# Performance work log

Hardware: AMD Instinct MI355X
Metric: run time of the kernel (lower is better)

## Reference

```python
import jax, jax.numpy as jnp
import numpy as np

B, T, N, CIN, H, K, HOR = 64, 12, 800, 2, 64, 3, 12
TCOV_IN, TCOV_H, MNUM, MDIM = 60, 2, 4, 8
KAPPA = 0.05
IN0 = CIN + TCOV_H  # layer-0 input dim: data channels + time-covariate embedding


def setup_inputs() -> dict:
    key = jax.random.key(0)
    ks = jax.random.split(key, 24)
    def nrm(k, shape, s=0.1):
        return jax.random.normal(k, shape, jnp.float32) * s
    inp = {}
    inp["x_seq"] = jax.random.normal(ks[0], (B, T, N, CIN), jnp.float32)
    inp["t_x"] = jax.random.normal(ks[1], (B, T, TCOV_IN), jnp.float32)
    inp["t_y"] = jax.random.normal(ks[2], (B, HOR, TCOV_IN), jnp.float32)
    # adaptive graph as in init_adp_graph: softmax(relu(v1 @ v2), axis=1)
    inp["G"] = jax.nn.softmax(jax.nn.relu(nrm(ks[3], (N, 20), 1.0) @ nrm(ks[4], (20, N), 1.0)), axis=1)
    i = 5
    for pre in ("enc", "dec"):
        for l, hin in enumerate((IN0, H)):
            inp[f"{pre}_Wg{l}"] = nrm(ks[i], ((hin + H) * K, 2 * H)); i += 1
            inp[f"{pre}_bg{l}"] = jnp.zeros((2 * H,), jnp.float32)
            inp[f"{pre}_Wc{l}"] = nrm(ks[i], ((hin + H) * K, H)); i += 1
            inp[f"{pre}_bc{l}"] = jnp.zeros((H,), jnp.float32)
    inp["mlp_W1"] = nrm(ks[i], (TCOV_IN, 10)); i += 1
    inp["mlp_b1"] = jnp.zeros((10,), jnp.float32)
    inp["mlp_W2"] = nrm(ks[i], (10, TCOV_H * N)); i += 1
    inp["mlp_b2"] = jnp.zeros((TCOV_H * N,), jnp.float32)
    inp["memory"] = nrm(ks[i], (MNUM, MDIM), 1.0); i += 1
    inp["Wa"] = nrm(ks[i], (N * H, MDIM), 0.01); i += 1
    inp["fc"] = nrm(ks[i], (MDIM, MDIM * N), 0.1); i += 1
    inp["proj_W"] = nrm(ks[i], (H + MDIM, CIN)); i += 1
    inp["proj_b"] = jnp.zeros((CIN,), jnp.float32)
    return inp


def _cheby(G):
    # Chebyshev basis T_0..T_{K-1}: T_0=I, T_1=G, T_k = 2 G T_{k-1} - T_{k-2}
    Gs = [jnp.eye(N, dtype=G.dtype), G]
    for _ in range(2, K):
        Gs.append(2.0 * (G @ Gs[-1]) - Gs[-2])
    return jnp.stack(Gs[:K])  # (K, N, N)


def _gconv(x, Gs, W, b):
    # mixhop: h_k = kappa*x + (1-kappa) * einsum('bnp,nm->bmp', x, T_k); concat over k, then project
    agg = KAPPA * x[None] + (1.0 - KAPPA) * jnp.einsum('bnp,knm->kbmp', x, Gs)  # (K,B,N,P)
    Bq, Nq, P = x.shape
    h = jnp.transpose(agg, (1, 2, 0, 3)).reshape(Bq, Nq, K * P)  # matches torch.cat order
    return h @ W + b


def _cell(x, h, Gs, Wg, bg, Wc, bc):
    # GCRU cell: graph-conv GRU
    ur = _gconv(jnp.concatenate([x, h], -1), Gs, Wg, bg)
    u, r = jnp.split(ur, 2, axis=-1)
    u = jax.nn.sigmoid(u)
    r = jax.nn.sigmoid(r)
    c = jnp.tanh(_gconv(jnp.concatenate([x, r * h], -1), Gs, Wc, bc))
    return (1.0 - u) * h + u * c


def _mlp(t, W1, b1, W2, b2):
    # nn.Sequential(Linear, Linear) -- no activation in between
    return (t @ W1 + b1) @ W2 + b2


def reference(x_seq, t_x, t_y, G, enc_Wg0, enc_bg0, enc_Wc0, enc_bc0, enc_Wg1, enc_bg1, enc_Wc1, enc_bc1, dec_Wg0, dec_bg0, dec_Wc0, dec_bc0, dec_Wg1, dec_bg1, dec_Wc1, dec_bc1, mlp_W1, mlp_b1, mlp_W2, mlp_b2, memory, Wa, fc, proj_W, proj_b):
    Gs = _cheby(G)
    # time covariates for encoder input
    tx_emb = _mlp(t_x, mlp_W1, mlp_b1, mlp_W2, mlp_b2).reshape(B, T, N, TCOV_H)
    x = jnp.concatenate([x_seq, tx_emb], -1)  # (B,T,N,IN0)
    # encoder: scan over time per layer
    seq = jnp.swapaxes(x, 0, 1)  # (T,B,N,.)
    enc_params = [(enc_Wg0, enc_bg0, enc_Wc0, enc_bc0), (enc_Wg1, enc_bg1, enc_Wc1, enc_bc1)]
    h_last = []
    for (Wg, bg, Wc, bc) in enc_params:
        def step(h, xt, Wg=Wg, bg=bg, Wc=Wc, bc=bc):
            hn = _cell(xt, h, Gs, Wg, bg, Wc, bc)
            return hn, hn
        h0 = jnp.zeros((B, N, H), x.dtype)
        hT, seq = jax.lax.scan(step, h0, seq)
        h_last.append(hT)
    dec_params = [(dec_Wg0, dec_bg0, dec_Wc0, dec_bc0), (dec_Wg1, dec_bg1, dec_Wc1, dec_bc1)]
    ty = jnp.swapaxes(t_y, 0, 1)  # (HOR,B,TCOV_IN)

    def dec_step(carry, tyt):
        go, h0, h1 = carry
        tye = _mlp(tyt, mlp_W1, mlp_b1, mlp_W2, mlp_b2).reshape(B, N, TCOV_H)
        xin = jnp.concatenate([go, tye], -1)
        h0 = _cell(xin, h0, Gs, *dec_params[0])
        h1 = _cell(h0, h1, Gs, *dec_params[1])
        # query_st_memory
        q = h1.reshape(B, N * H) @ Wa  # (B, MDIM)
        att = jax.nn.softmax(q @ memory.T, axis=1)  # (B, MNUM)
        attm = ((att @ memory) @ fc).reshape(B, N, MDIM)
        out = jax.nn.relu(jnp.concatenate([h1, attm], -1) @ proj_W + proj_b)  # (B,N,CIN)
        return (out, h0, h1), out

    go0 = jnp.zeros((B, N, CIN), x.dtype)
    _, outs = jax.lax.scan(dec_step, (go0, h_last[0], h_last[1]), ty)
    return jnp.swapaxes(outs, 0, 1)  # (B,HOR,N,CIN)
```

## Files before the change

### kernel.cpp

```cpp
#include <hip/hip_runtime.h>
#include <math.h>

typedef _Float16 f16_t;
typedef _Float16 half8 __attribute__((ext_vector_type(8)));
typedef float f32x4 __attribute__((ext_vector_type(4)));


struct Params {
  const float *x_seq, *t_x, *t_y, *G;
  const float *Wraw[8], *bia[8];
  const float *mW1, *mb1, *mW2, *mb2, *mem, *Wa, *fc, *projW, *projb;
  float* dout;
  float *h0, *h1, *txe, *tye, *hidb, *partial, *Wat;
  f16_t *T2h, *Bpk, *Y0g, *Ybg, *Y0c, *Ybc, *Uh;
  f16_t* wsp[8];
};

__device__ __forceinline__ float sigm(float x) { return 1.0f / (1.0f + expf(-x)); }

__device__ __forceinline__ int xcd_swz(int orig, int nwg) {
  int q = nwg >> 3, r = nwg & 7, xcd = orig & 7, j = orig >> 3;
  return (xcd < r ? xcd * (q + 1) : r * (q + 1) + (xcd - r) * q) + j;
}

__device__ __forceinline__ void gload16(const void* g, void* l) {
  __builtin_amdgcn_global_load_lds((const __attribute__((address_space(1))) void*)g,
                                   (__attribute__((address_space(3))) void*)l, 16, 0, 0);
}


__global__ void __launch_bounds__(256) k_pre0(Params p) {
  int nt = gridDim.x * blockDim.x, id = blockIdx.x * blockDim.x + threadIdx.x;
  float4 z = {0.f, 0.f, 0.f, 0.f};
  for (int i = id; i < 64 * 64 * 200; i += nt) { ((float4*)p.h0)[i] = z; ((float4*)p.h1)[i] = z; }
  for (int w = 0; w < 8; ++w) {
    int layer = (w >> 1) & 1, cand = w & 1;
    int P = layer ? 128 : 68, NC = cand ? 64 : 128;
    const float* W = p.Wraw[w];
    f16_t* dst = p.wsp[w];
    int tot = 3 * NC * 128;
    for (int idx = id; idx < tot; idx += nt) {
      int s = idx / (NC * 128), rem = idx - s * (NC * 128);
      int c = rem >> 7, pp = rem & 127;
      float v = 0.f;
      if (pp < P) {
        if (s == 0)
          v = W[(size_t)pp * NC + c] + 0.05f * (W[(size_t)(P + pp) * NC + c] + W[(size_t)(2 * P + pp) * NC + c]);
        else
          v = 0.95f * W[(size_t)(s * P + pp) * NC + c];
      }
      dst[idx] = (f16_t)v;
    }
  }
  for (int idx = id; idx < 15360; idx += nt) {
    int half = idx / 7680, rem = idx - half * 7680;
    int r = rem / 10, j = rem - r * 10;
    const float* tin = half ? p.t_y : p.t_x;
    float a = p.mb1[j];
    for (int k = 0; k < 60; ++k) a += tin[(size_t)r * 60 + k] * p.mW1[k * 10 + j];
    p.hidb[idx] = a;
  }
  for (int idx = id; idx < 409600; idx += nt) {
    int c = idx / 6400, r2 = idx - c * 6400;
    int n = r2 >> 3, d = r2 & 7;
    p.Wat[idx] = p.Wa[((size_t)n * 64 + c) * 8 + d];
  }
}

__global__ void __launch_bounds__(256) k_pre1(Params p) {
  __shared__ float As[16 * 68];
  __shared__ float Bs[16 * 68];
  int tid = threadIdx.x, tx = tid & 15, ty = tid >> 4;
  const float* A = p.G;
  for (int tile = blockIdx.x; tile < 169; tile += gridDim.x) {
    int bx = tile % 13, by = tile / 13;
    int rowBase = by * 64, colBase = bx * 64;
    float acc[4][4] = {};
    for (int k0 = 0; k0 < 800; k0 += 16) {
      __syncthreads();
      for (int e = tid; e < 1024; e += 256) {
        int r = e >> 4, c = e & 15;
        int gr = rowBase + r;
        As[c * 68 + r] = (gr < 800) ? A[gr * 800 + k0 + c] : 0.f;
      }
      for (int e = tid; e < 1024; e += 256) {
        int r = e >> 6, c = e & 63;
        int gc = colBase + c;
        Bs[r * 68 + c] = (gc < 800) ? A[(k0 + r) * 800 + gc] : 0.f;
      }
      __syncthreads();
#pragma unroll
      for (int kk = 0; kk < 16; ++kk) {
        float4 a4 = *(const float4*)&As[kk * 68 + ty * 4];
        float4 b4 = *(const float4*)&Bs[kk * 68 + tx * 4];
        float av[4] = {a4.x, a4.y, a4.z, a4.w};
        float bv[4] = {b4.x, b4.y, b4.z, b4.w};
#pragma unroll
        for (int i = 0; i < 4; ++i)
#pragma unroll
          for (int j = 0; j < 4; ++j) acc[i][j] += av[i] * bv[j];
      }
    }
#pragma unroll
    for (int i = 0; i < 4; ++i) {
      int m = rowBase + ty * 4 + i;
      if (m >= 800) continue;
#pragma unroll
      for (int j = 0; j < 4; ++j) {
        int n = colBase + tx * 4 + j;
        if (n < 800) p.T2h[(size_t)m * 800 + n] = (f16_t)(2.f * acc[i][j] - (m == n ? 1.f : 0.f));
      }
    }
  }
  int nt = gridDim.x * blockDim.x, id = blockIdx.x * blockDim.x + threadIdx.x;
  for (int idx = id; idx < 2 * 768 * 1600; idx += nt) {
    int half = idx / (768 * 1600), rem = idx - half * (768 * 1600);
    int r = rem / 1600, o = rem - r * 1600;
    const float* hid = p.hidb + half * 7680;
    float* emb = half ? p.tye : p.txe;
    float a = p.mb2[o];
#pragma unroll
    for (int k = 0; k < 10; ++k) a += hid[r * 10 + k] * p.mW2[k * 1600 + o];
    emb[rem] = a;
  }
}

__global__ void __launch_bounds__(256) k_pre2(Params p) {
  int nt = gridDim.x * blockDim.x, id = blockIdx.x * blockDim.x + threadIdx.x;
  for (int idx = id; idx < 7 * 50 * 4096; idx += nt) {
    int nT = idx / 204800, rem = idx - nT * 204800;
    int ks = rem >> 12, i = rem & 4095;
    int kg = i >> 10, col = (i >> 3) & 127, e = i & 7;
    int k = ks * 32 + kg * 8 + e;
    int n = nT * 128 + col;
    f16_t v = (f16_t)0.f;
    if (n < 800) v = (k < 800) ? (f16_t)p.G[(size_t)k * 800 + n] : p.T2h[(size_t)(k - 800) * 800 + n];
    p.Bpk[idx] = v;
  }
}

template <int LAYER>
__global__ void __launch_bounds__(256, 3) g_small(Params p, int widx, int dec, int t) {
  __shared__ f16_t XS[128 * 136];
  unsigned* XS32 = (unsigned*)XS;
  int tid = threadIdx.x, lane = tid & 63, wid = tid >> 6;
  int lrow = lane & 15, lgrp = lane >> 4;
  int wm = wid >> 1, wn = wid & 1;
  int swz = xcd_swz(blockIdx.x, gridDim.x);
  int b = swz / 7, nBase = (swz % 7) * 128;
  const f16_t* __restrict__ wb = p.wsp[widx];
  const float* emb = dec ? p.tye : p.txe;

  {
    int rp = tid >> 3, n0 = (tid & 7) * 16;
    int ng = nBase + n0;
    bool nval = ng < 800;
    for (int pass = 0; pass < 2; ++pass) {
      float v[2][16];
#pragma unroll
      for (int par = 0; par < 2; ++par) {
        int cp = pass * 64 + 2 * rp + par;
        float* vv = v[par];
        if (!nval) {
#pragma unroll
          for (int i = 0; i < 16; ++i) vv[i] = 0.f;
        } else if (LAYER == 1) {
          const float* src = (cp < 64) ? p.h0 + ((size_t)(b * 64 + cp)) * 800 + ng
                                       : p.h1 + ((size_t)(b * 64 + cp - 64)) * 800 + ng;
#pragma unroll
          for (int q = 0; q < 4; ++q) {
            float4 f = *(const float4*)(src + q * 4);
            vv[q * 4 + 0] = f.x; vv[q * 4 + 1] = f.y; vv[q * 4 + 2] = f.z; vv[q * 4 + 3] = f.w;
          }
        } else {
          if (cp >= 68) {
#pragma unroll
            for (int i = 0; i < 16; ++i) vv[i] = 0.f;
          } else if (cp >= 4) {
            const float* src = p.h0 + ((size_t)(b * 64 + cp - 4)) * 800 + ng;
#pragma unroll
            for (int q = 0; q < 4; ++q) {
              float4 f = *(const float4*)(src + q * 4);
              vv[q * 4 + 0] = f.x; vv[q * 4 + 1] = f.y; vv[q * 4 + 2] = f.z; vv[q * 4 + 3] = f.w;
            }
          } else if (cp >= 2) {
#pragma unroll
            for (int i = 0; i < 16; ++i)
              vv[i] = emb[(size_t)(b * 12 + t) * 1600 + (ng + i) * 2 + (cp - 2)];
          } else {
            if (dec) {
              if (t == 0) {
#pragma unroll
                for (int i = 0; i < 16; ++i) vv[i] = 0.f;
              } else {
#pragma unroll
                for (int i = 0; i < 16; ++i)
                  vv[i] = p.dout[((size_t)(b * 12 + t - 1) * 800 + ng + i) * 2 + cp];
              }
            } else {
#pragma unroll
              for (int i = 0; i < 16; ++i)
                vv[i] = p.x_seq[((size_t)(b * 12 + t) * 800 + ng + i) * 2 + cp];
            }
          }
        }
      }
#pragma unroll
      for (int i = 0; i < 16; ++i) {
        union { f16_t h[2]; unsigned u; } pk;
        pk.h[0] = (f16_t)v[0][i];
        pk.h[1] = (f16_t)v[1][i];
        XS32[(n0 + i) * 68 + pass * 32 + rp] = pk.u;
      }
    }
  }
  __syncthreads();

  for (int s = 0; s < 3; ++s) {
    f32x4 acc[4][4];
#pragma unroll
    for (int i = 0; i < 4; ++i)
#pragma unroll
      for (int j = 0; j < 4; ++j) acc[i][j] = (f32x4){0.f, 0.f, 0.f, 0.f};
#pragma unroll
    for (int ks = 0; ks < 4; ++ks) {
      half8 fa[4], fx[4];
#pragma unroll
      for (int mf = 0; mf < 4; ++mf)
        fa[mf] = *(const half8*)(wb + ((size_t)(s * 128 + wm * 64 + mf * 16 + lrow) << 7) + ks * 32 + lgrp * 8);
#pragma unroll
      for (int nt = 0; nt < 4; ++nt)
        fx[nt] = *(const half8*)(XS + (wn * 64 + nt * 16 + lrow) * 136 + ks * 32 + lgrp * 8);
#pragma unroll
      for (int mf = 0; mf < 4; ++mf)
#pragma unroll
        for (int nt = 0; nt < 4; ++nt)
          acc[mf][nt] = __builtin_amdgcn_mfma_f32_16x16x32_f16(fa[mf], fx[nt], acc[mf][nt], 0, 0, 0);
    }
#pragma unroll
    for (int mf = 0; mf < 4; ++mf)
#pragma unroll
      for (int nt = 0; nt < 4; ++nt) {
        int n = nBase + wn * 64 + nt * 16 + lrow;
        if (n >= 800) continue;
#pragma unroll
        for (int j = 0; j < 4; ++j) {
          int c = wm * 64 + mf * 16 + lgrp * 4 + j;
          size_t r = (size_t)(b * 128 + c);
          f16_t val = (f16_t)acc[mf][nt][j];
          if (s == 0) {
            p.Y0g[r * 800 + n] = val;
          } else {
            int kp = (s - 1) * 800 + n;
            p.Ybg[((size_t)(kp >> 3) * 8192 + r) * 8 + (kp & 7)] = val;
          }
        }
      }
  }
}

template <int LAYER>
__global__ void __launch_bounds__(256, 4) g_biggate(Params p, int w0, int dec, int t, float* hcur) {
  constexpr int Pin = LAYER ? 64 : 4;
  __shared__ __align__(16) f16_t SH[18432];
  f16_t* AS = SH;
  f16_t* BS = SH + 6144;
  int tid = threadIdx.x, lane = tid & 63, w = tid >> 6;
  int lrow = lane & 15, lgrp = lane >> 4;
  int wm = w >> 1, wn = w & 1;
  int swz = xcd_swz(blockIdx.x, gridDim.x);
  int rt = swz / 7;
  int rBase = rt * 64;
  int nTile = swz % 7;
  int b = rt >> 1;
  int rhblk = rt & 1;
  const f16_t* __restrict__ Abase = p.Ybg;
  const f16_t* __restrict__ Bbase = p.Bpk + (size_t)nTile * 204800;
  const float* bias = p.bia[w0];

  auto stage = [&](int buf, int ks) {
    gload16(Abase + ((size_t)(ks * 4 + w) * 8192 + rBase + lane) * 8, AS + buf * 2048 + w * 512);
    gload16(Bbase + (size_t)ks * 4096 + (size_t)(w * 2 + 0) * 512 + lane * 8, BS + buf * 4096 + (w * 2 + 0) * 512);
    gload16(Bbase + (size_t)ks * 4096 + (size_t)(w * 2 + 1) * 512 + lane * 8, BS + buf * 4096 + (w * 2 + 1) * 512);
  };

  f32x4 acc[2][4];
#pragma unroll
  for (int i = 0; i < 2; ++i)
#pragma unroll
    for (int j = 0; j < 4; ++j) acc[i][j] = (f32x4){0.f, 0.f, 0.f, 0.f};

  stage(0, 0);
  stage(1, 1);
  for (int ks = 0; ks < 50; ++ks) {
    if (ks == 49) {
      asm volatile("s_waitcnt vmcnt(0)" ::: "memory");
    } else {
      asm volatile("s_waitcnt vmcnt(3)" ::: "memory");
    }
    __builtin_amdgcn_s_barrier();
    __builtin_amdgcn_sched_barrier(0);
    if (ks + 2 < 50) stage((ks + 2) % 3, ks + 2);
    int cur = ks % 3;
    half8 fa[2], fb[4];
#pragma unroll
    for (int mt = 0; mt < 2; ++mt)
      fa[mt] = *(const half8*)(AS + cur * 2048 + lgrp * 512 + (wm * 32 + mt * 16 + lrow) * 8);
#pragma unroll
    for (int nt = 0; nt < 4; ++nt)
      fb[nt] = *(const half8*)(BS + cur * 4096 + lgrp * 1024 + (wn * 64 + nt * 16 + lrow) * 8);
#pragma unroll
    for (int mt = 0; mt < 2; ++mt)
#pragma unroll
      for (int nt = 0; nt < 4; ++nt)
        acc[mt][nt] = __builtin_amdgcn_mfma_f32_16x16x32_f16(fa[mt], fb[nt], acc[mt][nt], 0, 0, 0);
  }

  if (!rhblk) {
#pragma unroll
    for (int mt = 0; mt < 2; ++mt)
#pragma unroll
      for (int nt = 0; nt < 4; ++nt) {
        int n = nTile * 128 + wn * 64 + nt * 16 + lrow;
        if (n >= 800) continue;
#pragma unroll
        for (int j = 0; j < 4; ++j) {
          int c = wm * 32 + mt * 16 + lgrp * 4 + j;
          int r = rBase + c;
          float v = acc[mt][nt][j] + (float)p.Y0g[(size_t)r * 800 + n] + bias[c];
          p.Uh[(size_t)(b * 64 + c) * 800 + n] = (f16_t)sigm(v);
        }
      }
    return;
  }

  f16_t rhv[2][4][4];
#pragma unroll
  for (int mt = 0; mt < 2; ++mt)
#pragma unroll
    for (int nt = 0; nt < 4; ++nt) {
      int n = nTile * 128 + wn * 64 + nt * 16 + lrow;
#pragma unroll
      for (int j = 0; j < 4; ++j) {
        int jj = wm * 32 + mt * 16 + lgrp * 4 + j;
        if (n < 800) {
          int r = rBase + jj;
          float v = acc[mt][nt][j] + (float)p.Y0g[(size_t)r * 800 + n] + bias[64 + jj];
          float hv = hcur[(size_t)(b * 64 + jj) * 800 + n];
          rhv[mt][nt][j] = (f16_t)(sigm(v) * hv);
        } else {
          rhv[mt][nt][j] = (f16_t)0.f;
        }
      }
    }

  __syncthreads();
  f16_t* Xc = SH;

#pragma unroll
  for (int mt = 0; mt < 2; ++mt)
#pragma unroll
    for (int nt = 0; nt < 4; ++nt) {
      int col = wn * 64 + nt * 16 + lrow;
#pragma unroll
      for (int j = 0; j < 4; ++j) {
        int jj = wm * 32 + mt * 16 + lgrp * 4 + j;
        Xc[col * 136 + Pin + jj] = rhv[mt][nt][j];
      }
    }
  if (LAYER == 1) {
    int ct = tid >> 2, nq = tid & 3;
    const float* src = p.h0 + (size_t)(b * 64 + ct) * 800;
#pragma unroll 8
    for (int i = 0; i < 32; ++i) {
      int nl = nq * 32 + i;
      int n = nTile * 128 + nl;
      float v = (n < 800) ? src[n] : 0.f;
      Xc[nl * 136 + ct] = (f16_t)v;
    }
  } else {
    if (tid < 128) {
      int col = tid;
      int n = nTile * 128 + col;
      float v0 = 0.f, v1 = 0.f, v2 = 0.f, v3 = 0.f;
      if (n < 800) {
        if (dec) {
          if (t > 0) {
            v0 = p.dout[((size_t)(b * 12 + t - 1) * 800 + n) * 2 + 0];
            v1 = p.dout[((size_t)(b * 12 + t - 1) * 800 + n) * 2 + 1];
          }
        } else {
          v0 = p.x_seq[((size_t)(b * 12 + t) * 800 + n) * 2 + 0];
          v1 = p.x_seq[((size_t)(b * 12 + t) * 800 + n) * 2 + 1];
        }
        const float* emb = dec ? p.tye : p.txe;
        v2 = emb[(size_t)(b * 12 + t) * 1600 + n * 2 + 0];
        v3 = emb[(size_t)(b * 12 + t) * 1600 + n * 2 + 1];
      }
      Xc[col * 136 + 0] = (f16_t)v0;
      Xc[col * 136 + 1] = (f16_t)v1;
      Xc[col * 136 + 2] = (f16_t)v2;
      Xc[col * 136 + 3] = (f16_t)v3;
      unsigned* z32 = (unsigned*)(Xc + col * 136 + 68);
#pragma unroll
      for (int q = 0; q < 30; ++q) z32[q] = 0u;
    }
  }
  __syncthreads();

  const f16_t* __restrict__ wc = p.wsp[w0 + 1];
  int cwn = w;
  for (int s = 0; s < 3; ++s) {
    f32x4 ac[4][2];
#pragma unroll
    for (int i = 0; i < 4; ++i)
#pragma unroll
      for (int j = 0; j < 2; ++j) ac[i][j] = (f32x4){0.f, 0.f, 0.f, 0.f};
#pragma unroll
    for (int ks = 0; ks < 4; ++ks) {
      half8 fa[4], fx[2];
#pragma unroll
      for (int mf = 0; mf < 4; ++mf)
        fa[mf] = *(const half8*)(wc + ((size_t)(s * 64 + mf * 16 + lrow) << 7) + ks * 32 + lgrp * 8);
#pragma unroll
      for (int nt = 0; nt < 2; ++nt)
        fx[nt] = *(const half8*)(Xc + (cwn * 32 + nt * 16 + lrow) * 136 + ks * 32 + lgrp * 8);
#pragma unroll
      for (int mf = 0; mf < 4; ++mf)
#pragma unroll
        for (int nt = 0; nt < 2; ++nt)
          ac[mf][nt] = __builtin_amdgcn_mfma_f32_16x16x32_f16(fa[mf], fx[nt], ac[mf][nt], 0, 0, 0);
    }
#pragma unroll
    for (int mf = 0; mf < 4; ++mf)
#pragma unroll
      for (int nt = 0; nt < 2; ++nt) {
        int n = nTile * 128 + cwn * 32 + nt * 16 + lrow;
        if (n >= 800) continue;
#pragma unroll
        for (int j = 0; j < 4; ++j) {
          int c = mf * 16 + lgrp * 4 + j;
          size_t r = (size_t)(b * 64 + c);
          f16_t val = (f16_t)ac[mf][nt][j];
          if (s == 0) {
            p.Y0c[r * 800 + n] = val;
          } else {
            int kp = (s - 1) * 800 + n;
            p.Ybc[((size_t)(kp >> 3) * 4096 + r) * 8 + (kp & 7)] = val;
          }
        }
      }
  }
}

__global__ void __launch_bounds__(256, 4) g_bigcand(Params p, int widx, float* hcur) {
  __shared__ __align__(16) f16_t SH[18432];
  f16_t* AS = SH;
  f16_t* BS = SH + 6144;
  int tid = threadIdx.x, lane = tid & 63, w = tid >> 6;
  int lrow = lane & 15, lgrp = lane >> 4;
  int wm = w >> 1, wn = w & 1;
  int swz = xcd_swz(blockIdx.x, gridDim.x);
  int rBase = (swz / 7) * 64;
  int nTile = swz % 7;
  const f16_t* __restrict__ Abase = p.Ybc;
  const f16_t* __restrict__ Bbase = p.Bpk + (size_t)nTile * 204800;
  const float* bias = p.bia[widx];

  auto stage = [&](int buf, int ks) {
    gload16(Abase + ((size_t)(ks * 4 + w) * 4096 + rBase + lane) * 8, AS + buf * 2048 + w * 512);
    gload16(Bbase + (size_t)ks * 4096 + (size_t)(w * 2 + 0) * 512 + lane * 8, BS + buf * 4096 + (w * 2 + 0) * 512);
    gload16(Bbase + (size_t)ks * 4096 + (size_t)(w * 2 + 1) * 512 + lane * 8, BS + buf * 4096 + (w * 2 + 1) * 512);
  };

  f32x4 acc[2][4];
#pragma unroll
  for (int i = 0; i < 2; ++i)
#pragma unroll
    for (int j = 0; j < 4; ++j) acc[i][j] = (f32x4){0.f, 0.f, 0.f, 0.f};

  stage(0, 0);
  stage(1, 1);
  for (int ks = 0; ks < 50; ++ks) {
    if (ks == 49) {
      asm volatile("s_waitcnt vmcnt(0)" ::: "memory");
    } else {
      asm volatile("s_waitcnt vmcnt(3)" ::: "memory");
    }
    __builtin_amdgcn_s_barrier();
    __builtin_amdgcn_sched_barrier(0);
    if (ks + 2 < 50) stage((ks + 2) % 3, ks + 2);
    int cur = ks % 3;
    half8 fa[2], fb[4];
#pragma unroll
    for (int mt = 0; mt < 2; ++mt)
      fa[mt] = *(const half8*)(AS + cur * 2048 + lgrp * 512 + (wm * 32 + mt * 16 + lrow) * 8);
#pragma unroll
    for (int nt = 0; nt < 4; ++nt)
      fb[nt] = *(const half8*)(BS + cur * 4096 + lgrp * 1024 + (wn * 64 + nt * 16 + lrow) * 8);
#pragma unroll
    for (int mt = 0; mt < 2; ++mt)
#pragma unroll
      for (int nt = 0; nt < 4; ++nt)
        acc[mt][nt] = __builtin_amdgcn_mfma_f32_16x16x32_f16(fa[mt], fb[nt], acc[mt][nt], 0, 0, 0);
  }

#pragma unroll
  for (int mt = 0; mt < 2; ++mt)
#pragma unroll
    for (int nt = 0; nt < 4; ++nt) {
      int n = nTile * 128 + wn * 64 + nt * 16 + lrow;
      if (n >= 800) continue;
#pragma unroll
      for (int j = 0; j < 4; ++j) {
        int r = rBase + wm * 32 + mt * 16 + lgrp * 4 + j;
        int b = r >> 6, c = r & 63;
        float v = acc[mt][nt][j] + (float)p.Y0c[(size_t)r * 800 + n] + bias[c];
        float u = (float)p.Uh[(size_t)(b * 64 + c) * 800 + n];
        float hv = hcur[(size_t)(b * 64 + c) * 800 + n];
        hcur[(size_t)(b * 64 + c) * 800 + n] = (1.f - u) * hv + u * tanhf(v);
      }
    }
}


__global__ void __launch_bounds__(256) k_att1(Params p) {
  int gwid = (blockIdx.x * blockDim.x + threadIdx.x) >> 6;
  int nw = (gridDim.x * blockDim.x) >> 6;
  int lane = threadIdx.x & 63;
  for (int tile = gwid; tile < 1024; tile += nw) {
    int cx = tile & 15, b = tile >> 4;
    float acc[8] = {};
    const float* hrow = p.h1 + (size_t)b * 51200 + cx * 3200;
    const float* wbase = p.Wat + (size_t)cx * 3200 * 8;
    for (int i = lane; i < 3200; i += 64) {
      float hv = hrow[i];
      const float* wr = wbase + (size_t)i * 8;
#pragma unroll
      for (int j = 0; j < 8; ++j) acc[j] += hv * wr[j];
    }
#pragma unroll
    for (int s = 1; s < 64; s <<= 1) {
#pragma unroll
      for (int j = 0; j < 8; ++j) acc[j] += __shfl_xor(acc[j], s);
    }
    if (lane == 0) {
#pragma unroll
      for (int j = 0; j < 8; ++j) p.partial[((size_t)b * 16 + cx) * 8 + j] = acc[j];
    }
  }
}

__global__ void __launch_bounds__(256) k_att2(Params p, int t) {
  int b = blockIdx.x >> 2, q4 = blockIdx.x & 3;
  int tid = threadIdx.x;
  float qv[8] = {};
  for (int cx = 0; cx < 16; ++cx)
#pragma unroll
    for (int j = 0; j < 8; ++j) qv[j] += p.partial[((size_t)b * 16 + cx) * 8 + j];
  float sco[4], mx = -1e30f;
#pragma unroll
  for (int m = 0; m < 4; ++m) {
    float s = 0.f;
#pragma unroll
    for (int d = 0; d < 8; ++d) s += qv[d] * p.mem[m * 8 + d];
    sco[m] = s;
    mx = fmaxf(mx, s);
  }
  float se = 0.f;
#pragma unroll
  for (int m = 0; m < 4; ++m) { sco[m] = expf(sco[m] - mx); se += sco[m]; }
  float attv[8];
#pragma unroll
  for (int d = 0; d < 8; ++d) {
    float av = 0.f;
#pragma unroll
    for (int m = 0; m < 4; ++m) av += (sco[m] / se) * p.mem[m * 8 + d];
    attv[d] = av;
  }
  if (tid >= 200) return;
  int n = q4 * 200 + tid;
  float attm[8];
#pragma unroll
  for (int d = 0; d < 8; ++d) {
    float s = 0.f;
#pragma unroll
    for (int m = 0; m < 8; ++m) s += attv[m] * p.fc[(size_t)m * 6400 + n * 8 + d];
    attm[d] = s;
  }
  float o0 = p.projb[0], o1 = p.projb[1];
  const float* hb = p.h1 + (size_t)b * 51200 + n;
#pragma unroll 16
  for (int j = 0; j < 64; ++j) {
    float hv = hb[(size_t)j * 800];
    o0 += hv * p.projW[j * 2 + 0];
    o1 += hv * p.projW[j * 2 + 1];
  }
#pragma unroll
  for (int d = 0; d < 8; ++d) {
    o0 += attm[d] * p.projW[(64 + d) * 2 + 0];
    o1 += attm[d] * p.projW[(64 + d) * 2 + 1];
  }
  size_t base = ((size_t)(b * 12 + t) * 800 + n) * 2;
  p.dout[base + 0] = fmaxf(o0, 0.f);
  p.dout[base + 1] = fmaxf(o1, 0.f);
}


extern "C" void kernel_launch(void* const* d_in, const int* in_sizes, int n_in,
                              void* d_out, int out_size, void* d_ws, size_t ws_size,
                              hipStream_t stream) {
  Params P;
  P.x_seq = (const float*)d_in[0];
  P.t_x = (const float*)d_in[1];
  P.t_y = (const float*)d_in[2];
  P.G = (const float*)d_in[3];
  P.Wraw[0] = (const float*)d_in[4];  P.bia[0] = (const float*)d_in[5];
  P.Wraw[1] = (const float*)d_in[6];  P.bia[1] = (const float*)d_in[7];
  P.Wraw[2] = (const float*)d_in[8];  P.bia[2] = (const float*)d_in[9];
  P.Wraw[3] = (const float*)d_in[10]; P.bia[3] = (const float*)d_in[11];
  P.Wraw[4] = (const float*)d_in[12]; P.bia[4] = (const float*)d_in[13];
  P.Wraw[5] = (const float*)d_in[14]; P.bia[5] = (const float*)d_in[15];
  P.Wraw[6] = (const float*)d_in[16]; P.bia[6] = (const float*)d_in[17];
  P.Wraw[7] = (const float*)d_in[18]; P.bia[7] = (const float*)d_in[19];
  P.mW1 = (const float*)d_in[20];
  P.mb1 = (const float*)d_in[21];
  P.mW2 = (const float*)d_in[22];
  P.mb2 = (const float*)d_in[23];
  P.mem = (const float*)d_in[24];
  P.Wa = (const float*)d_in[25];
  P.fc = (const float*)d_in[26];
  P.projW = (const float*)d_in[27];
  P.projb = (const float*)d_in[28];
  P.dout = (float*)d_out;

  float* ws = (float*)d_ws;
  size_t off = 0;
  auto alloc = [&](size_t nel) { float* q = ws + off; off += (nel + 3) & ~(size_t)3; return q; };
  P.T2h = (f16_t*)alloc(320000);
  P.Bpk = (f16_t*)alloc((size_t)7 * 50 * 4096 / 2);
  P.Y0g = (f16_t*)alloc((size_t)8192 * 800 / 2);
  P.Ybg = (f16_t*)alloc((size_t)1600 * 8192 / 2);
  P.Y0c = (f16_t*)alloc((size_t)4096 * 800 / 2);
  P.Ybc = (f16_t*)alloc((size_t)1600 * 4096 / 2);
  P.Uh = (f16_t*)alloc((size_t)4096 * 800 / 2);
  P.h0 = alloc((size_t)4096 * 800);
  P.h1 = alloc((size_t)4096 * 800);
  P.txe = alloc((size_t)768 * 1600);
  P.tye = alloc((size_t)768 * 1600);
  P.hidb = alloc(15360);
  P.partial = alloc(8192);
  P.Wat = alloc(409600);
  for (int w = 0; w < 8; ++w) {
    int cand = w & 1;
    int NC = cand ? 64 : 128;
    P.wsp[w] = (f16_t*)alloc((size_t)3 * NC * 128 / 2);
  }

  k_pre0<<<512, 256, 0, stream>>>(P);
  k_pre1<<<512, 256, 0, stream>>>(P);
  k_pre2<<<512, 256, 0, stream>>>(P);

  auto cell = [&](int dec, int t) {
    int w0 = dec * 4;
    g_small<0><<<448, 256, 0, stream>>>(P, w0 + 0, dec, t);
    g_biggate<0><<<896, 256, 0, stream>>>(P, w0 + 0, dec, t, P.h0);
    g_bigcand<<<448, 256, 0, stream>>>(P, w0 + 1, P.h0);
    g_small<1><<<448, 256, 0, stream>>>(P, w0 + 2, dec, t);
    g_biggate<1><<<896, 256, 0, stream>>>(P, w0 + 2, dec, t, P.h1);
    g_bigcand<<<448, 256, 0, stream>>>(P, w0 + 3, P.h1);
  };

  for (int t = 0; t < 12; ++t) cell(0, t);
  for (int t = 0; t < 12; ++t) {
    cell(1, t);
    k_att1<<<256, 256, 0, stream>>>(P);
    k_att2<<<256, 256, 0, stream>>>(P, t);
  }
}
```

Baseline: 6.597 ms.

## Wavefront-pipeline encoder layers so layer 0 step s runs with layer 1 step s-1

Restructures the encoder schedule into a diagonal wavefront. Each launch now runs layer 0 at time s and layer 1 at time s-1 together, with the block index selecting the layer, and intermediate buffers are duplicated per layer so the two can run concurrently. This halves the number of encoder launches and doubles the grid size per launch, which is meant to cut launch and tail overhead and raise occupancy. The cost is double the workspace for intermediates and kernels that branch on the block index.

```diff
diff --git a/kernel.cpp b/kernel.cpp
--- a/kernel.cpp
+++ b/kernel.cpp
@@ -12,7 +12,8 @@
   const float *mW1, *mb1, *mW2, *mb2, *mem, *Wa, *fc, *projW, *projb;
   float* dout;
   float *h0, *h1, *txe, *tye, *hidb, *partial, *Wat;
-  f16_t *T2h, *Bpk, *Y0g, *Ybg, *Y0c, *Ybc, *Uh;
+  f16_t *T2h, *Bpk;
+  f16_t *Y0gL[2], *YbgL[2], *Y0cL[2], *YbcL[2], *UhL[2];
   f16_t* wsp[8];
 };
 
@@ -140,13 +141,14 @@
 }
 
 template <int LAYER>
-__global__ void __launch_bounds__(256, 3) g_small(Params p, int widx, int dec, int t) {
-  __shared__ f16_t XS[128 * 136];
-  unsigned* XS32 = (unsigned*)XS;
+__device__ void small_body(const Params& p, char* smraw, int widx, int dec, int t,
+                           f16_t* __restrict__ Y0g, f16_t* __restrict__ Ybg, int lblk) {
+  f16_t* XS = (f16_t*)smraw;
+  unsigned* XS32 = (unsigned*)smraw;
   int tid = threadIdx.x, lane = tid & 63, wid = tid >> 6;
   int lrow = lane & 15, lgrp = lane >> 4;
   int wm = wid >> 1, wn = wid & 1;
-  int swz = xcd_swz(blockIdx.x, gridDim.x);
+  int swz = xcd_swz(lblk, 448);
   int b = swz / 7, nBase = (swz % 7) * 128;
   const f16_t* __restrict__ wb = p.wsp[widx];
   const float* emb = dec ? p.tye : p.txe;
@@ -249,10 +251,10 @@
           size_t r = (size_t)(b * 128 + c);
           f16_t val = (f16_t)acc[mf][nt][j];
           if (s == 0) {
-            p.Y0g[r * 800 + n] = val;
+            Y0g[r * 800 + n] = val;
           } else {
             int kp = (s - 1) * 800 + n;
-            p.Ybg[((size_t)(kp >> 3) * 8192 + r) * 8 + (kp & 7)] = val;
+            Ybg[((size_t)(kp >> 3) * 8192 + r) * 8 + (kp & 7)] = val;
           }
         }
       }
@@ -260,26 +262,28 @@
 }
 
 template <int LAYER>
-__global__ void __launch_bounds__(256, 4) g_biggate(Params p, int w0, int dec, int t, float* hcur) {
+__device__ void biggate_body(const Params& p, char* smraw, int w0, int dec, int t, float* hcur,
+                             const f16_t* __restrict__ Y0g, const f16_t* __restrict__ Ybg,
+                             f16_t* __restrict__ Y0c, f16_t* __restrict__ Ybc,
+                             f16_t* __restrict__ Uh, int lblk) {
   constexpr int Pin = LAYER ? 64 : 4;
-  __shared__ __align__(16) f16_t SH[18432];
+  f16_t* SH = (f16_t*)smraw;
   f16_t* AS = SH;
   f16_t* BS = SH + 6144;
   int tid = threadIdx.x, lane = tid & 63, w = tid >> 6;
   int lrow = lane & 15, lgrp = lane >> 4;
   int wm = w >> 1, wn = w & 1;
-  int swz = xcd_swz(blockIdx.x, gridDim.x);
+  int swz = xcd_swz(lblk, 896);
   int rt = swz / 7;
   int rBase = rt * 64;
   int nTile = swz % 7;
   int b = rt >> 1;
   int rhblk = rt & 1;
-  const f16_t* __restrict__ Abase = p.Ybg;
   const f16_t* __restrict__ Bbase = p.Bpk + (size_t)nTile * 204800;
   const float* bias = p.bia[w0];
 
   auto stage = [&](int buf, int ks) {
-    gload16(Abase + ((size_t)(ks * 4 + w) * 8192 + rBase + lane) * 8, AS + buf * 2048 + w * 512);
+    gload16(Ybg + ((size_t)(ks * 4 + w) * 8192 + rBase + lane) * 8, AS + buf * 2048 + w * 512);
     gload16(Bbase + (size_t)ks * 4096 + (size_t)(w * 2 + 0) * 512 + lane * 8, BS + buf * 4096 + (w * 2 + 0) * 512);
     gload16(Bbase + (size_t)ks * 4096 + (size_t)(w * 2 + 1) * 512 + lane * 8, BS + buf * 4096 + (w * 2 + 1) * 512);
   };
@@ -327,8 +331,8 @@
         for (int j = 0; j < 4; ++j) {
           int c = wm * 32 + mt * 16 + lgrp * 4 + j;
           int r = rBase + c;
-          float v = acc[mt][nt][j] + (float)p.Y0g[(size_t)r * 800 + n] + bias[c];
-          p.Uh[(size_t)(b * 64 + c) * 800 + n] = (f16_t)sigm(v);
+          float v = acc[mt][nt][j] + (float)Y0g[(size_t)r * 800 + n] + bias[c];
+          Uh[(size_t)(b * 64 + c) * 800 + n] = (f16_t)sigm(v);
         }
       }
     return;
@@ -345,7 +349,7 @@
         int jj = wm * 32 + mt * 16 + lgrp * 4 + j;
         if (n < 800) {
           int r = rBase + jj;
-          float v = acc[mt][nt][j] + (float)p.Y0g[(size_t)r * 800 + n] + bias[64 + jj];
+          float v = acc[mt][nt][j] + (float)Y0g[(size_t)r * 800 + n] + bias[64 + jj];
           float hv = hcur[(size_t)(b * 64 + jj) * 800 + n];
           rhv[mt][nt][j] = (f16_t)(sigm(v) * hv);
         } else {
@@ -443,32 +447,33 @@
           size_t r = (size_t)(b * 64 + c);
           f16_t val = (f16_t)ac[mf][nt][j];
           if (s == 0) {
-            p.Y0c[r * 800 + n] = val;
+            Y0c[r * 800 + n] = val;
           } else {
             int kp = (s - 1) * 800 + n;
-            p.Ybc[((size_t)(kp >> 3) * 4096 + r) * 8 + (kp & 7)] = val;
+            Ybc[((size_t)(kp >> 3) * 4096 + r) * 8 + (kp & 7)] = val;
           }
         }
       }
   }
 }
 
-__global__ void __launch_bounds__(256, 4) g_bigcand(Params p, int widx, float* hcur) {
-  __shared__ __align__(16) f16_t SH[18432];
+__device__ void bigcand_body(const Params& p, char* smraw, int widx, float* hcur,
+                             const f16_t* __restrict__ Y0c, const f16_t* __restrict__ Ybc,
+                             const f16_t* __restrict__ Uh, int lblk) {
+  f16_t* SH = (f16_t*)smraw;
   f16_t* AS = SH;
   f16_t* BS = SH + 6144;
   int tid = threadIdx.x, lane = tid & 63, w = tid >> 6;
   int lrow = lane & 15, lgrp = lane >> 4;
   int wm = w >> 1, wn = w & 1;
-  int swz = xcd_swz(blockIdx.x, gridDim.x);
+  int swz = xcd_swz(lblk, 448);
   int rBase = (swz / 7) * 64;
   int nTile = swz % 7;
-  const f16_t* __restrict__ Abase = p.Ybc;
   const f16_t* __restrict__ Bbase = p.Bpk + (size_t)nTile * 204800;
   const float* bias = p.bia[widx];
 
   auto stage = [&](int buf, int ks) {
-    gload16(Abase + ((size_t)(ks * 4 + w) * 4096 + rBase + lane) * 8, AS + buf * 2048 + w * 512);
+    gload16(Ybc + ((size_t)(ks * 4 + w) * 4096 + rBase + lane) * 8, AS + buf * 2048 + w * 512);
     gload16(Bbase + (size_t)ks * 4096 + (size_t)(w * 2 + 0) * 512 + lane * 8, BS + buf * 4096 + (w * 2 + 0) * 512);
     gload16(Bbase + (size_t)ks * 4096 + (size_t)(w * 2 + 1) * 512 + lane * 8, BS + buf * 4096 + (w * 2 + 1) * 512);
   };
@@ -515,12 +520,52 @@
       for (int j = 0; j < 4; ++j) {
         int r = rBase + wm * 32 + mt * 16 + lgrp * 4 + j;
         int b = r >> 6, c = r & 63;
-        float v = acc[mt][nt][j] + (float)p.Y0c[(size_t)r * 800 + n] + bias[c];
-        float u = (float)p.Uh[(size_t)(b * 64 + c) * 800 + n];
+        float v = acc[mt][nt][j] + (float)Y0c[(size_t)r * 800 + n] + bias[c];
+        float u = (float)Uh[(size_t)(b * 64 + c) * 800 + n];
         float hv = hcur[(size_t)(b * 64 + c) * 800 + n];
         hcur[(size_t)(b * 64 + c) * 800 + n] = (1.f - u) * hv + u * tanhf(v);
       }
     }
+}
+
+
+template <int LAYER>
+__global__ void __launch_bounds__(256, 3) s_one(Params p, int widx, int dec, int t) {
+  __shared__ __align__(16) char sm[34816];
+  small_body<LAYER>(p, sm, widx, dec, t, p.Y0gL[LAYER], p.YbgL[LAYER], blockIdx.x);
+}
+__global__ void __launch_bounds__(256, 3) s_both(Params p, int t0, int t1) {
+  __shared__ __align__(16) char sm[34816];
+  if (blockIdx.x < 448)
+    small_body<0>(p, sm, 0, 0, t0, p.Y0gL[0], p.YbgL[0], blockIdx.x);
+  else
+    small_body<1>(p, sm, 2, 0, t1, p.Y0gL[1], p.YbgL[1], blockIdx.x - 448);
+}
+
+template <int LAYER>
+__global__ void __launch_bounds__(256, 4) gg_one(Params p, int w0, int dec, int t) {
+  __shared__ __align__(16) char sm[36864];
+  biggate_body<LAYER>(p, sm, w0, dec, t, LAYER ? p.h1 : p.h0, p.Y0gL[LAYER], p.YbgL[LAYER],
+                      p.Y0cL[LAYER], p.YbcL[LAYER], p.UhL[LAYER], blockIdx.x);
+}
+__global__ void __launch_bounds__(256, 4) gg_both(Params p, int t0, int t1) {
+  __shared__ __align__(16) char sm[36864];
+  if (blockIdx.x < 896)
+    biggate_body<0>(p, sm, 0, 0, t0, p.h0, p.Y0gL[0], p.YbgL[0], p.Y0cL[0], p.YbcL[0], p.UhL[0], blockIdx.x);
+  else
+    biggate_body<1>(p, sm, 2, 0, t1, p.h1, p.Y0gL[1], p.YbgL[1], p.Y0cL[1], p.YbcL[1], p.UhL[1], blockIdx.x - 896);
+}
+
+__global__ void __launch_bounds__(256, 4) gc_one(Params p, int widx, int layer) {
+  __shared__ __align__(16) char sm[36864];
+  bigcand_body(p, sm, widx, layer ? p.h1 : p.h0, p.Y0cL[layer], p.YbcL[layer], p.UhL[layer], blockIdx.x);
+}
+__global__ void __launch_bounds__(256, 4) gc_both(Params p) {
+  __shared__ __align__(16) char sm[36864];
+  if (blockIdx.x < 448)
+    bigcand_body(p, sm, 1, p.h0, p.Y0cL[0], p.YbcL[0], p.UhL[0], blockIdx.x);
+  else
+    bigcand_body(p, sm, 3, p.h1, p.Y0cL[1], p.YbcL[1], p.UhL[1], blockIdx.x - 448);
 }
 
 
@@ -639,11 +684,13 @@
   auto alloc = [&](size_t nel) { float* q = ws + off; off += (nel + 3) & ~(size_t)3; return q; };
   P.T2h = (f16_t*)alloc(320000);
   P.Bpk = (f16_t*)alloc((size_t)7 * 50 * 4096 / 2);
-  P.Y0g = (f16_t*)alloc((size_t)8192 * 800 / 2);
-  P.Ybg = (f16_t*)alloc((size_t)1600 * 8192 / 2);
-  P.Y0c = (f16_t*)alloc((size_t)4096 * 800 / 2);
-  P.Ybc = (f16_t*)alloc((size_t)1600 * 4096 / 2);
-  P.Uh = (f16_t*)alloc((size_t)4096 * 800 / 2);
+  for (int l = 0; l < 2; ++l) {
+    P.Y0gL[l] = (f16_t*)alloc((size_t)8192 * 800 / 2);
+    P.YbgL[l] = (f16_t*)alloc((size_t)1600 * 8192 / 2);
+    P.Y0cL[l] = (f16_t*)alloc((size_t)4096 * 800 / 2);
+    P.YbcL[l] = (f16_t*)alloc((size_t)1600 * 4096 / 2);
+    P.UhL[l] = (f16_t*)alloc((size_t)4096 * 800 / 2);
+  }
   P.h0 = alloc((size_t)4096 * 800);
   P.h1 = alloc((size_t)4096 * 800);
   P.txe = alloc((size_t)768 * 1600);
@@ -661,19 +708,25 @@
   k_pre1<<<512, 256, 0, stream>>>(P);
   k_pre2<<<512, 256, 0, stream>>>(P);
 
-  auto cell = [&](int dec, int t) {
-    int w0 = dec * 4;
-    g_small<0><<<448, 256, 0, stream>>>(P, w0 + 0, dec, t);
-    g_biggate<0><<<896, 256, 0, stream>>>(P, w0 + 0, dec, t, P.h0);
-    g_bigcand<<<448, 256, 0, stream>>>(P, w0 + 1, P.h0);
-    g_small<1><<<448, 256, 0, stream>>>(P, w0 + 2, dec, t);
-    g_biggate<1><<<896, 256, 0, stream>>>(P, w0 + 2, dec, t, P.h1);
-    g_bigcand<<<448, 256, 0, stream>>>(P, w0 + 3, P.h1);
-  };
-
-  for (int t = 0; t < 12; ++t) cell(0, t);
+  s_one<0><<<448, 256, 0, stream>>>(P, 0, 0, 0);
+  gg_one<0><<<896, 256, 0, stream>>>(P, 0, 0, 0);
+  gc_one<<<448, 256, 0, stream>>>(P, 1, 0);
+  for (int s = 1; s <= 11; ++s) {
+    s_both<<<896, 256, 0, stream>>>(P, s, s - 1);
+    gg_both<<<1792, 256, 0, stream>>>(P, s, s - 1);
+    gc_both<<<896, 256, 0, stream>>>(P);
+  }
+  s_one<1><<<448, 256, 0, stream>>>(P, 2, 0, 11);
+  gg_one<1><<<896, 256, 0, stream>>>(P, 2, 0, 11);
+  gc_one<<<448, 256, 0, stream>>>(P, 3, 1);
+
   for (int t = 0; t < 12; ++t) {
-    cell(1, t);
+    s_one<0><<<448, 256, 0, stream>>>(P, 4, 1, t);
+    gg_one<0><<<896, 256, 0, stream>>>(P, 4, 1, t);
+    gc_one<<<448, 256, 0, stream>>>(P, 5, 0);
+    s_one<1><<<448, 256, 0, stream>>>(P, 6, 1, t);
+    gg_one<1><<<896, 256, 0, stream>>>(P, 6, 1, t);
+    gc_one<<<448, 256, 0, stream>>>(P, 7, 1);
     k_att1<<<256, 256, 0, stream>>>(P);
     k_att2<<<256, 256, 0, stream>>>(P, t);
   }
```

Result: no change. 6.471 ms, median of 2 (-1.9%).
